# Performance work log

Measured on AMD Instinct MI355X. Metric: run time of the kernel, lower is better.

Reference implementation:

```python
import jax, jax.numpy as jnp
import numpy as np
from jax import lax

N = 2048
B = 8
CH = 10
START = 1
STOP = 65


def setup_inputs() -> dict:
    key = jax.random.key(0)
    ks = jax.random.split(key, 13)

    def g(k, s):
        return jax.random.normal(k, s, jnp.float32) * 0.05

    return {
        "x": jax.random.normal(ks[0], (B, 1, N, N), jnp.float32),
        "wl": g(ks[1], (CH // 2, 1, 3, N)), "bl": g(ks[2], (CH // 2,)),
        "wr": g(ks[3], (CH // 2, 1, N, 3)), "br": g(ks[4], (CH // 2,)),
        "wA": g(ks[5], (CH, CH, 3)), "bA": g(ks[6], (CH,)),
        "wB": g(ks[7], (CH, CH, 3)), "bB": g(ks[8], (CH,)),  # shared by layers 2&3 (torch list aliasing)
        "wT": g(ks[9], (CH, CH, 3)), "bT": g(ks[10], (CH,)),
        "wm": g(ks[11], (2, CH, 1)), "bm": g(ks[12], (2,)),
        "start": START, "stop": STOP,
    }


def _conv1d(h, w, b, pad):
    y = lax.conv_general_dilated(h, w, (1,), [(pad, pad)], dimension_numbers=("NCH", "OIH", "NCH"))
    return y + b[None, :, None]


def _forward(x, wl, bl, wr, br, wA, bA, wB, bB, wT, bT, wm, bm, start, stop):
    n = x.shape[-1]
    # scan_left: Conv2d kernel (3, n), padding (1, 0) -> (B, 5, n, 1) -> squeeze
    left_ = lax.conv_general_dilated(x, wl, (1, 1), [(1, 1), (0, 0)], dimension_numbers=("NCHW", "OIHW", "NCHW"))
    left_ = left_[..., 0] + bl[None, :, None]
    # scan_right: Conv2d kernel (n, 3), padding (0, 1) -> (B, 5, 1, n) -> squeeze
    right_ = lax.conv_general_dilated(x, wr, (1, 1), [(0, 0), (1, 1)], dimension_numbers=("NCHW", "OIHW", "NCHW"))
    right_ = right_[:, :, 0, :] + br[None, :, None]
    lr = jnp.concatenate([left_, right_], axis=1)  # (B, 10, n)
    h = jax.nn.relu(_conv1d(lr, wA, bA, 1))
    h = jax.nn.relu(_conv1d(h, wB, bB, 1))  # same weights twice: torch [conv, relu]*2 aliasing
    h = jax.nn.relu(_conv1d(h, wB, bB, 1))
    # ConvTranspose1d(k=3, stride=1, pad=1) == Conv1d with transposed, spatially-flipped kernel, pad=1
    wTc = jnp.flip(jnp.swapaxes(wT, 0, 1), -1)
    for _ in range(3):
        h = jax.nn.relu(_conv1d(h, wTc, bT, 1))
    m = jax.nn.sigmoid(_conv1d(h, wm, bm, 0))  # (B, 2, n)
    left, right = m[:, 0, :], m[:, 1, :]
    xs = x[:, 0]  # (B, n, n)
    preds = []
    for d in range(start, stop):  # static diagonal indices
        curr = jnp.exp(jnp.diagonal(xs, offset=d, axis1=1, axis2=2))  # (B, n-d)
        mass_in = curr[:, 1:] * right[:, 1:n - d] + curr[:, :-1] * left[:, d:n - 1]
        mass_out = right[:, 0:n - d - 1] + left[:, d + 1:n]
        p = jnp.log(mass_in / mass_out)
        preds.append(p - jnp.mean(p))  # scalar mean over batch+positions, as torch.mean
    return jnp.concatenate(preds, axis=1)  # ragged preds concatenated: (B, sum(n-d-1))


def reference(x, wl, bl, wr, br, wA, bA, wB, bB, wT, bT, wm, bm, start, stop):
    return _forward(x, wl, bl, wr, br, wA, bA, wB, bB, wT, bT, wm, bm, start, stop)
```

## Files before the change

### kernel.cpp

```cpp
#include <hip/hip_runtime.h>
#include <hip/hip_bf16.h>

#define NN 2048
#define BB 8
#define TROW 128928

typedef __attribute__((ext_vector_type(8))) short bf16x8;
typedef __attribute__((ext_vector_type(4))) unsigned u32x4;
typedef __attribute__((ext_vector_type(4))) float f32x4;

__device__ __forceinline__ unsigned pk2(float lo, float hi) {
    float2 t; t.x = lo; t.y = hi;
    __hip_bfloat162 h = __float22bfloat162_rn(t);
    union { __hip_bfloat162 h; unsigned u; } c; c.h = h;
    return c.u;
}

__global__ __launch_bounds__(512, 2) void k_all(const float* __restrict__ x,
                                                const float* __restrict__ wl,
                                                const float* __restrict__ wr,
                                                const float* __restrict__ bl,
                                                const float* __restrict__ br,
                                                const float* __restrict__ wA, const float* __restrict__ bA,
                                                const float* __restrict__ wB, const float* __restrict__ bB,
                                                const float* __restrict__ wT, const float* __restrict__ bT,
                                                const float* __restrict__ wm, const float* __restrict__ bm,
                                                float* __restrict__ R,
                                                float* __restrict__ CS,
                                                float* __restrict__ LEFT, float* __restrict__ RIGHT,
                                                float* __restrict__ psum,
                                                int* __restrict__ counters,
                                                float* __restrict__ outp) {
    __shared__ float T[65][65];
    __shared__ float buf0[10][80], buf1[10][80];
    __shared__ float W[3][10][10][3];
    __shared__ float Bs[3][10];
    __shared__ float Wm[2][10], Bm[2];
    __shared__ float psl[64];
    __shared__ float lfs[132], rts[68];

    int blk = blockIdx.x;
    int tid = threadIdx.x;
    int b = blk >> 5;
    int rg = blk & 31;
    int i0 = rg << 6;

    if (tid < 256) {
        int wv = tid >> 6, lane = tid & 63;
        int q = lane >> 4, m = lane & 15;
        int r0 = rg * 64 + wv * 16;
        int nrow = (m == 15) ? 14 : m;

        const float* ap = x + ((size_t)(b * NN + r0 + m)) * NN + q * 8;
        const float* bp = wl + (size_t)nrow * NN + q * 8;

        f32x4 acc = {0.f, 0.f, 0.f, 0.f};
#pragma unroll 4
        for (int it = 0; it < 64; it++) {
            const float* a0 = ap + it * 32;
            const float* b0 = bp + it * 32;
            float4 av0 = *(const float4*)(a0);
            float4 av1 = *(const float4*)(a0 + 4);
            float4 bv0 = *(const float4*)(b0);
            float4 bv1 = *(const float4*)(b0 + 4);
            union { bf16x8 v; u32x4 u; } A, Bv;
            A.u[0] = pk2(av0.x, av0.y); A.u[1] = pk2(av0.z, av0.w);
            A.u[2] = pk2(av1.x, av1.y); A.u[3] = pk2(av1.z, av1.w);
            Bv.u[0] = pk2(bv0.x, bv0.y); Bv.u[1] = pk2(bv0.z, bv0.w);
            Bv.u[2] = pk2(bv1.x, bv1.y); Bv.u[3] = pk2(bv1.z, bv1.w);
            acc = __builtin_amdgcn_mfma_f32_16x16x32_bf16(A.v, Bv.v, acc, 0, 0, 0);
        }
        float* rp = R + ((size_t)b * NN + r0) * 16;
#pragma unroll
        for (int reg = 0; reg < 4; reg++)
            rp[(q * 4 + reg) * 16 + m] = acc[reg];
    } else {
        int t2 = tid - 256;
        int jc = rg >> 4, rc = rg & 15;
        int r0 = rc * 128;
        int c0 = jc * 1024 + t2 * 4;
        const float* xp = x + ((size_t)b * NN + r0) * NN + c0;

        float acc[15][4];
#pragma unroll
        for (int k = 0; k < 15; k++)
#pragma unroll
            for (int e = 0; e < 4; e++) acc[k][e] = 0.f;

        for (int rb = 0; rb < 16; rb++) {
            float4 xv[8];
#pragma unroll
            for (int q = 0; q < 8; q++)
                xv[q] = *(const float4*)(xp + (size_t)(rb * 8 + q) * NN);
#pragma unroll
            for (int q = 0; q < 8; q++) {
                int h = r0 + rb * 8 + q;
#pragma unroll
                for (int k = 0; k < 15; k++) {
                    int c = k / 3, dw = k - c * 3;
                    float wk = wr[c * (NN * 3) + h * 3 + dw];
                    acc[k][0] = fmaf(xv[q].x, wk, acc[k][0]);
                    acc[k][1] = fmaf(xv[q].y, wk, acc[k][1]);
                    acc[k][2] = fmaf(xv[q].z, wk, acc[k][2]);
                    acc[k][3] = fmaf(xv[q].w, wk, acc[k][3]);
                }
            }
        }
#pragma unroll
        for (int k = 0; k < 15; k++) {
            float* dst = CS + ((size_t)b * 16 + k) * NN + c0;
            atomicAdd(dst + 0, acc[k][0]);
            atomicAdd(dst + 1, acc[k][1]);
            atomicAdd(dst + 2, acc[k][2]);
            atomicAdd(dst + 3, acc[k][3]);
        }
    }
    __syncthreads();
    if (tid == 0) {
        __threadfence();
        atomicAdd(&counters[0], 1);
    }

    for (int idx = tid; idx < 900; idx += 512) {
        int set = idx / 300, rem = idx - set * 300;
        int o = rem / 30, rem2 = rem - o * 30, c = rem2 / 3, kk = rem2 - c * 3;
        float u;
        if (set == 0) u = wA[o * 30 + c * 3 + kk];
        else if (set == 1) u = wB[o * 30 + c * 3 + kk];
        else u = wT[c * 30 + o * 3 + (2 - kk)];
        W[set][o][c][kk] = u;
    }
    if (tid < 30) {
        float v = (tid < 10) ? bA[tid] : (tid < 20) ? bB[tid - 10] : bT[tid - 20];
        Bs[tid / 10][tid % 10] = v;
    }
    if (tid < 20) Wm[tid / 10][tid % 10] = wm[tid];
    if (tid < 2) Bm[tid] = bm[tid];

    for (int idx = tid; idx < 65 * 64; idx += 512) {
        int r = idx >> 6, dm1 = idx & 63;
        int row = i0 + r;
        int col = row + dm1 + 1;
        float v = 0.f;
        if (row < NN && col < NN) v = __expf(x[((size_t)b * NN + row) * NN + col]);
        T[r][dm1] = v;
    }

    if (tid == 0) {
        while (__hip_atomic_load(&counters[0], __ATOMIC_ACQUIRE, __HIP_MEMORY_SCOPE_AGENT) < 256) {
            __builtin_amdgcn_s_sleep(2);
        }
    }
    __syncthreads();

    for (int idx = tid; idx < 760; idx += 512) {
        int ch = idx / 76, p = idx - ch * 76;
        int g = i0 - 6 + p;
        float v = 0.f;
        if (g >= 0 && g < NN) {
            if (ch < 5) {
                v = bl[ch];
#pragma unroll
                for (int dh = 0; dh < 3; dh++) {
                    int r = g + dh - 1;
                    if (r >= 0 && r < NN)
                        v += __hip_atomic_load(&R[(size_t)(b * NN + r) * 16 + ch * 3 + dh],
                                               __ATOMIC_RELAXED, __HIP_MEMORY_SCOPE_AGENT);
                }
            } else {
                int c = ch - 5;
                v = br[c];
#pragma unroll
                for (int dw = 0; dw < 3; dw++) {
                    int j = g + dw - 1;
                    if (j >= 0 && j < NN)
                        v += __hip_atomic_load(&CS[((size_t)b * 16 + c * 3 + dw) * NN + j],
                                               __ATOMIC_RELAXED, __HIP_MEMORY_SCOPE_AGENT);
                }
            }
        }
        buf0[ch][p] = v;
    }
    __syncthreads();

    float(*in)[80] = buf0;
    float(*out)[80] = buf1;
    for (int layer = 0; layer < 6; layer++) {
        int set = (layer == 0) ? 0 : (layer < 3 ? 1 : 2);
        int lo = layer + 1;
        for (int idx = tid; idx < 760; idx += 512) {
            int o = idx / 76, p = idx - o * 76;
            if (p >= lo && p < 76 - lo) {
                float s = Bs[set][o];
#pragma unroll
                for (int c = 0; c < 10; c++) {
                    const float* ip = &in[c][p];
                    s = fmaf(ip[-1], W[set][o][c][0], s);
                    s = fmaf(ip[0], W[set][o][c][1], s);
                    s = fmaf(ip[1], W[set][o][c][2], s);
                }
                s = s > 0.f ? s : 0.f;
                int g = i0 - 6 + p;
                if (g < 0 || g >= NN) s = 0.f;
                out[o][p] = s;
            }
        }
        __syncthreads();
        float(*tmp)[80] = in; in = out; out = tmp;
    }

    if (tid < 128) {
        int o = tid >> 6, pp = tid & 63;
        int p = 6 + pp;
        float s = Bm[o];
#pragma unroll
        for (int c = 0; c < 10; c++) s = fmaf(in[c][p], Wm[o][c], s);
        float sig = 1.f / (1.f + __expf(-s));
        float* dst = (o ? RIGHT : LEFT) + b * NN + i0 + pp;
        __hip_atomic_store(dst, sig, __ATOMIC_RELAXED, __HIP_MEMORY_SCOPE_AGENT);
    }
    __syncthreads();

    if (tid == 0) {
        __threadfence();
        atomicAdd(&counters[1], 1);
        while (__hip_atomic_load(&counters[1], __ATOMIC_ACQUIRE, __HIP_MEMORY_SCOPE_AGENT) < 256) {
            __builtin_amdgcn_s_sleep(2);
        }
    }
    __syncthreads();

    if (tid < 195) {
        if (tid < 129) {
            int g = i0 + 1 + tid; if (g > NN - 1) g = NN - 1;
            lfs[tid] = __hip_atomic_load(LEFT + b * NN + g, __ATOMIC_RELAXED, __HIP_MEMORY_SCOPE_AGENT);
        } else {
            int p2 = tid - 129;
            int g = i0 + p2; if (g > NN - 1) g = NN - 1;
            rts[p2] = __hip_atomic_load(RIGHT + b * NN + g, __ATOMIC_RELAXED, __HIP_MEMORY_SCOPE_AGENT);
        }
    }
    __syncthreads();

    int wv = tid >> 6, lane = tid & 63;
    int i = i0 + lane;
    float pv[8];
#pragma unroll
    for (int s = 0; s < 8; s++) {
        int dm1 = wv * 8 + s;
        int d = dm1 + 1;
        int L = (NN - 1) - d;
        float p = 0.f;
        if (i < L) {
            float mi = T[lane + 1][dm1] * rts[lane + 1] + T[lane][dm1] * lfs[dm1 + lane];
            float mo = rts[lane] + lfs[dm1 + lane + 1];
            p = __logf(mi / mo);
        }
        pv[s] = p;
        float s64 = p;
        for (int off = 32; off; off >>= 1) s64 += __shfl_down(s64, off);
        if (lane == 0) psl[dm1] = s64;
    }
    __syncthreads();
    if (tid < 64) atomicAdd(&psum[tid], psl[tid]);
    __syncthreads();

    if (tid == 0) {
        __threadfence();
        atomicAdd(&counters[2], 1);
        while (__hip_atomic_load(&counters[2], __ATOMIC_ACQUIRE, __HIP_MEMORY_SCOPE_AGENT) < 256) {
            __builtin_amdgcn_s_sleep(2);
        }
    }
    __syncthreads();
    if (tid < 64)
        psl[tid] = __hip_atomic_load(&psum[tid], __ATOMIC_RELAXED, __HIP_MEMORY_SCOPE_AGENT);
    __syncthreads();

#pragma unroll
    for (int s = 0; s < 8; s++) {
        int dm1 = wv * 8 + s;
        int d = dm1 + 1;
        int L = (NN - 1) - d;
        if (i < L) {
            float mean = psl[dm1] / (float)(8 * L);
            size_t off0 = (size_t)dm1 * (NN - 1) - (size_t)dm1 * (dm1 + 1) / 2;
            outp[(size_t)b * TROW + off0 + i] = pv[s] - mean;
        }
    }
}

extern "C" void kernel_launch(void* const* d_in, const int* in_sizes, int n_in,
                              void* d_out, int out_size, void* d_ws, size_t ws_size,
                              hipStream_t stream) {
    const float* x = (const float*)d_in[0];
    const float* wl = (const float*)d_in[1];
    const float* bl = (const float*)d_in[2];
    const float* wr = (const float*)d_in[3];
    const float* br = (const float*)d_in[4];
    const float* wA = (const float*)d_in[5];
    const float* bA = (const float*)d_in[6];
    const float* wB = (const float*)d_in[7];
    const float* bB = (const float*)d_in[8];
    const float* wT = (const float*)d_in[9];
    const float* bT = (const float*)d_in[10];
    const float* wm = (const float*)d_in[11];
    const float* bm = (const float*)d_in[12];

    float* ws = (float*)d_ws;
    float* R     = ws;
    float* LEFT  = ws + 262144;
    float* RIGHT = ws + 278528;
    float* CS    = ws + 294912;
    float* psum  = ws + 557056;
    int*   counters = (int*)(ws + 557120);

    hipMemsetAsync(ws + 294912, 0, (size_t)(262144 + 64 + 4) * 4, stream);

    k_all<<<256, 512, 0, stream>>>(x, wl, wr, bl, br, wA, bA, wB, bB, wT, bT, wm, bm,
                                   R, CS, LEFT, RIGHT, psum, counters, (float*)d_out);
}
```

Measured before the change: 330.8 us.

## Recompute conv halos per block in LDS to drop a grid barrier and global atomics

Each block now computes its own row-convolution partials (80 rows including halo) and column-scan partials (80 columns over all rows) into shared memory. This replaces the global R/CS buffers, the atomicAdd column reduction, the large memset and one grid-wide spin barrier. The diagonal exp tile is now loaded after the LEFT/RIGHT store, which overlaps it with the remaining barrier. In exchange, x is partly read redundantly across neighbouring blocks. The column pass is also a long serial loop of strided scalar loads per wave, which may be latency-bound.

```diff
diff --git a/kernel.cpp b/kernel.cpp
--- a/kernel.cpp
+++ b/kernel.cpp
@@ -25,101 +25,27 @@
                                                 const float* __restrict__ wB, const float* __restrict__ bB,
                                                 const float* __restrict__ wT, const float* __restrict__ bT,
                                                 const float* __restrict__ wm, const float* __restrict__ bm,
-                                                float* __restrict__ R,
-                                                float* __restrict__ CS,
                                                 float* __restrict__ LEFT, float* __restrict__ RIGHT,
                                                 float* __restrict__ psum,
                                                 int* __restrict__ counters,
                                                 float* __restrict__ outp) {
-    __shared__ float T[65][65];
     __shared__ float buf0[10][80], buf1[10][80];
     __shared__ float W[3][10][10][3];
     __shared__ float Bs[3][10];
     __shared__ float Wm[2][10], Bm[2];
     __shared__ float psl[64];
     __shared__ float lfs[132], rts[68];
-
-    int blk = blockIdx.x;
-    int tid = threadIdx.x;
-    int b = blk >> 5;
-    int rg = blk & 31;
-    int i0 = rg << 6;
-
-    if (tid < 256) {
-        int wv = tid >> 6, lane = tid & 63;
-        int q = lane >> 4, m = lane & 15;
-        int r0 = rg * 64 + wv * 16;
-        int nrow = (m == 15) ? 14 : m;
-
-        const float* ap = x + ((size_t)(b * NN + r0 + m)) * NN + q * 8;
-        const float* bp = wl + (size_t)nrow * NN + q * 8;
-
-        f32x4 acc = {0.f, 0.f, 0.f, 0.f};
-#pragma unroll 4
-        for (int it = 0; it < 64; it++) {
-            const float* a0 = ap + it * 32;
-            const float* b0 = bp + it * 32;
-            float4 av0 = *(const float4*)(a0);
-            float4 av1 = *(const float4*)(a0 + 4);
-            float4 bv0 = *(const float4*)(b0);
-            float4 bv1 = *(const float4*)(b0 + 4);
-            union { bf16x8 v; u32x4 u; } A, Bv;
-            A.u[0] = pk2(av0.x, av0.y); A.u[1] = pk2(av0.z, av0.w);
-            A.u[2] = pk2(av1.x, av1.y); A.u[3] = pk2(av1.z, av1.w);
-            Bv.u[0] = pk2(bv0.x, bv0.y); Bv.u[1] = pk2(bv0.z, bv0.w);
-            Bv.u[2] = pk2(bv1.x, bv1.y); Bv.u[3] = pk2(bv1.z, bv1.w);
-            acc = __builtin_amdgcn_mfma_f32_16x16x32_bf16(A.v, Bv.v, acc, 0, 0, 0);
-        }
-        float* rp = R + ((size_t)b * NN + r0) * 16;
-#pragma unroll
-        for (int reg = 0; reg < 4; reg++)
-            rp[(q * 4 + reg) * 16 + m] = acc[reg];
-    } else {
-        int t2 = tid - 256;
-        int jc = rg >> 4, rc = rg & 15;
-        int r0 = rc * 128;
-        int c0 = jc * 1024 + t2 * 4;
-        const float* xp = x + ((size_t)b * NN + r0) * NN + c0;
-
-        float acc[15][4];
-#pragma unroll
-        for (int k = 0; k < 15; k++)
-#pragma unroll
-            for (int e = 0; e < 4; e++) acc[k][e] = 0.f;
-
-        for (int rb = 0; rb < 16; rb++) {
-            float4 xv[8];
-#pragma unroll
-            for (int q = 0; q < 8; q++)
-                xv[q] = *(const float4*)(xp + (size_t)(rb * 8 + q) * NN);
-#pragma unroll
-            for (int q = 0; q < 8; q++) {
-                int h = r0 + rb * 8 + q;
-#pragma unroll
-                for (int k = 0; k < 15; k++) {
-                    int c = k / 3, dw = k - c * 3;
-                    float wk = wr[c * (NN * 3) + h * 3 + dw];
-                    acc[k][0] = fmaf(xv[q].x, wk, acc[k][0]);
-                    acc[k][1] = fmaf(xv[q].y, wk, acc[k][1]);
-                    acc[k][2] = fmaf(xv[q].z, wk, acc[k][2]);
-                    acc[k][3] = fmaf(xv[q].w, wk, acc[k][3]);
-                }
-            }
-        }
-#pragma unroll
-        for (int k = 0; k < 15; k++) {
-            float* dst = CS + ((size_t)b * 16 + k) * NN + c0;
-            atomicAdd(dst + 0, acc[k][0]);
-            atomicAdd(dst + 1, acc[k][1]);
-            atomicAdd(dst + 2, acc[k][2]);
-            atomicAdd(dst + 3, acc[k][3]);
-        }
-    }
-    __syncthreads();
-    if (tid == 0) {
-        __threadfence();
-        atomicAdd(&counters[0], 1);
-    }
+    __shared__ __align__(16) char upool[48640];
+    float (*Rloc)[80][16] = (float (*)[80][16])(upool);
+    float (*colp)[80][15] = (float (*)[80][15])(upool + 10240);
+    float (*T)[65]        = (float (*)[65])(upool);
+
+    const int tid = threadIdx.x;
+    const int b   = blockIdx.x >> 5;
+    const int rg  = blockIdx.x & 31;
+    const int i0  = rg << 6;
+    const int w   = __builtin_amdgcn_readfirstlane(tid >> 6);
+    const int lane = tid & 63;
 
     for (int idx = tid; idx < 900; idx += 512) {
         int set = idx / 300, rem = idx - set * 300;
@@ -137,18 +63,66 @@
     if (tid < 20) Wm[tid / 10][tid % 10] = wm[tid];
     if (tid < 2) Bm[tid] = bm[tid];
 
-    for (int idx = tid; idx < 65 * 64; idx += 512) {
-        int r = idx >> 6, dm1 = idx & 63;
-        int row = i0 + r;
-        int col = row + dm1 + 1;
-        float v = 0.f;
-        if (row < NN && col < NN) v = __expf(x[((size_t)b * NN + row) * NN + col]);
-        T[r][dm1] = v;
-    }
-
-    if (tid == 0) {
-        while (__hip_atomic_load(&counters[0], __ATOMIC_ACQUIRE, __HIP_MEMORY_SCOPE_AGENT) < 256) {
-            __builtin_amdgcn_s_sleep(2);
+    {
+        const int q = lane >> 4, m = lane & 15;
+        const int nrow = (m == 15) ? 14 : m;
+        for (int rep = 0; rep < 2; rep++) {
+            int job = rep ? (w < 2 ? 8 + w : -1) : w;
+            if (job < 0) break;
+            int grp = job % 5, kh = job / 5;
+            int rl = i0 - 8 + grp * 16 + m;
+            rl = rl < 0 ? 0 : (rl > NN - 1 ? NN - 1 : rl);
+            const float* ap = x + ((size_t)(b * NN + rl)) * NN + kh * 1024 + q * 8;
+            const float* bp = wl + (size_t)nrow * NN + kh * 1024 + q * 8;
+            f32x4 acc = {0.f, 0.f, 0.f, 0.f};
+#pragma unroll 4
+            for (int it = 0; it < 32; it++) {
+                const float* a0 = ap + it * 32;
+                const float* b0 = bp + it * 32;
+                float4 av0 = *(const float4*)(a0);
+                float4 av1 = *(const float4*)(a0 + 4);
+                float4 bv0 = *(const float4*)(b0);
+                float4 bv1 = *(const float4*)(b0 + 4);
+                union { bf16x8 v; u32x4 u; } A, Bv;
+                A.u[0] = pk2(av0.x, av0.y); A.u[1] = pk2(av0.z, av0.w);
+                A.u[2] = pk2(av1.x, av1.y); A.u[3] = pk2(av1.z, av1.w);
+                Bv.u[0] = pk2(bv0.x, bv0.y); Bv.u[1] = pk2(bv0.z, bv0.w);
+                Bv.u[2] = pk2(bv1.x, bv1.y); Bv.u[3] = pk2(bv1.z, bv1.w);
+                acc = __builtin_amdgcn_mfma_f32_16x16x32_bf16(A.v, Bv.v, acc, 0, 0, 0);
+            }
+#pragma unroll
+            for (int reg = 0; reg < 4; reg++)
+                Rloc[kh][grp * 16 + q * 4 + reg][m] = acc[reg];
+        }
+    }
+
+    {
+        int c1 = i0 - 7 + lane;  int c1c = c1 < 0 ? 0 : (c1 > NN - 1 ? NN - 1 : c1);
+        int c2 = i0 + 57 + lane; int c2c = c2 < 0 ? 0 : (c2 > NN - 1 ? NN - 1 : c2);
+        float a1[15], a2[15];
+#pragma unroll
+        for (int k = 0; k < 15; k++) { a1[k] = 0.f; a2[k] = 0.f; }
+        const float* xb = x + (size_t)b * NN * NN;
+        const int rbase = w * 256;
+        for (int it = 0; it < 256; it++) {
+            int r = rbase + it;
+            const float* xr = xb + (size_t)r * NN;
+            float v1 = xr[c1c];
+            float v2 = xr[c2c];
+            const float* wp = wr + r * 3;
+#pragma unroll
+            for (int k = 0; k < 15; k++) {
+                int c = k / 3, dw = k - c * 3;
+                float wk = wp[c * (NN * 3) + dw];
+                a1[k] = fmaf(v1, wk, a1[k]);
+                a2[k] = fmaf(v2, wk, a2[k]);
+            }
+        }
+#pragma unroll
+        for (int k = 0; k < 15; k++) colp[w][lane][k] = a1[k];
+        if (lane < 16) {
+#pragma unroll
+            for (int k = 0; k < 15; k++) colp[w][64 + lane][k] = a2[k];
         }
     }
     __syncthreads();
@@ -162,20 +136,25 @@
                 v = bl[ch];
 #pragma unroll
                 for (int dh = 0; dh < 3; dh++) {
-                    int r = g + dh - 1;
-                    if (r >= 0 && r < NN)
-                        v += __hip_atomic_load(&R[(size_t)(b * NN + r) * 16 + ch * 3 + dh],
-                                               __ATOMIC_RELAXED, __HIP_MEMORY_SCOPE_AGENT);
+                    int r = g - 1 + dh;
+                    if (r >= 0 && r < NN) {
+                        int rr = p + 1 + dh;
+                        v += Rloc[0][rr][ch * 3 + dh] + Rloc[1][rr][ch * 3 + dh];
+                    }
                 }
             } else {
                 int c = ch - 5;
                 v = br[c];
 #pragma unroll
                 for (int dw = 0; dw < 3; dw++) {
-                    int j = g + dw - 1;
-                    if (j >= 0 && j < NN)
-                        v += __hip_atomic_load(&CS[((size_t)b * 16 + c * 3 + dw) * NN + j],
-                                               __ATOMIC_RELAXED, __HIP_MEMORY_SCOPE_AGENT);
+                    int j = g - 1 + dw;
+                    if (j >= 0 && j < NN) {
+                        int ce = p + dw;
+                        float s = 0.f;
+#pragma unroll
+                        for (int ww = 0; ww < 8; ww++) s += colp[ww][ce][c * 3 + dw];
+                        v += s;
+                    }
                 }
             }
         }
@@ -223,8 +202,20 @@
 
     if (tid == 0) {
         __threadfence();
-        atomicAdd(&counters[1], 1);
-        while (__hip_atomic_load(&counters[1], __ATOMIC_ACQUIRE, __HIP_MEMORY_SCOPE_AGENT) < 256) {
+        atomicAdd(&counters[0], 1);
+    }
+
+    for (int idx = tid; idx < 65 * 64; idx += 512) {
+        int r = idx >> 6, dm1 = idx & 63;
+        int row = i0 + r;
+        int col = row + dm1 + 1;
+        float v = 0.f;
+        if (row < NN && col < NN) v = __expf(x[((size_t)b * NN + row) * NN + col]);
+        T[r][dm1] = v;
+    }
+
+    if (tid == 0) {
+        while (__hip_atomic_load(&counters[0], __ATOMIC_ACQUIRE, __HIP_MEMORY_SCOPE_AGENT) < 256) {
             __builtin_amdgcn_s_sleep(2);
         }
     }
@@ -242,12 +233,11 @@
     }
     __syncthreads();
 
-    int wv = tid >> 6, lane = tid & 63;
     int i = i0 + lane;
     float pv[8];
 #pragma unroll
     for (int s = 0; s < 8; s++) {
-        int dm1 = wv * 8 + s;
+        int dm1 = w * 8 + s;
         int d = dm1 + 1;
         int L = (NN - 1) - d;
         float p = 0.f;
@@ -267,8 +257,8 @@
 
     if (tid == 0) {
         __threadfence();
-        atomicAdd(&counters[2], 1);
-        while (__hip_atomic_load(&counters[2], __ATOMIC_ACQUIRE, __HIP_MEMORY_SCOPE_AGENT) < 256) {
+        atomicAdd(&counters[1], 1);
+        while (__hip_atomic_load(&counters[1], __ATOMIC_ACQUIRE, __HIP_MEMORY_SCOPE_AGENT) < 256) {
             __builtin_amdgcn_s_sleep(2);
         }
     }
@@ -279,7 +269,7 @@
 
 #pragma unroll
     for (int s = 0; s < 8; s++) {
-        int dm1 = wv * 8 + s;
+        int dm1 = w * 8 + s;
         int d = dm1 + 1;
         int L = (NN - 1) - d;
         if (i < L) {
@@ -308,15 +298,13 @@
     const float* bm = (const float*)d_in[12];
 
     float* ws = (float*)d_ws;
-    float* R     = ws;
-    float* LEFT  = ws + 262144;
-    float* RIGHT = ws + 278528;
-    float* CS    = ws + 294912;
-    float* psum  = ws + 557056;
-    int*   counters = (int*)(ws + 557120);
-
-    hipMemsetAsync(ws + 294912, 0, (size_t)(262144 + 64 + 4) * 4, stream);
+    float* LEFT  = ws;
+    float* RIGHT = ws + 16384;
+    float* psum  = ws + 32768;
+    int*   counters = (int*)(ws + 32832);
+
+    hipMemsetAsync(ws + 32768, 0, (size_t)(64 + 4) * 4, stream);
 
     k_all<<<256, 512, 0, stream>>>(x, wl, wr, bl, br, wA, bA, wB, bB, wT, bT, wm, bm,
-                                   R, CS, LEFT, RIGHT, psum, counters, (float*)d_out);
+                                   LEFT, RIGHT, psum, counters, (float*)d_out);
 }
```

Measured after the change: 313.4 us. 1.06x faster.
